# Performance work log

Measured on AMD Instinct MI355X. Metric: run time of the kernel, lower is better.

## Reference

```python
import jax, jax.numpy as jnp
import numpy as np


def setup_inputs() -> dict:
    key = jax.random.key(0)
    kq, kk, kv = jax.random.split(key, 3)
    B, L, E = 16, 2048, 512
    return {
        "queries": jax.random.normal(kq, (B, L, E), dtype=jnp.float32),
        "keys": jax.random.normal(kk, (B, L, E), dtype=jnp.float32),
        "values": jax.random.normal(kv, (B, L, E), dtype=jnp.float32),
    }


def reference(queries, keys, values):
    # queries: [B, L, E], keys: [B, S, E], values: [B, S, D]; causal mask requires L == S
    B, L, E = queries.shape
    S = keys.shape[1]
    scale = 1.0 / np.float32(np.sqrt(E))  # self.scale is None -> 1/sqrt(E)
    scores = jnp.einsum('ble,bse->bls', queries, keys)  # [B, L, S]
    causal = jnp.triu(jnp.ones((L, S), dtype=bool), k=1)  # True above diagonal -> masked
    scores = jnp.where(causal, -jnp.inf, scores)
    A = jax.nn.softmax(scale * scores, axis=-1)  # dropout p=0.0 -> identity
    V = jnp.einsum('bls,bsd->bld', A, values)  # [B, L, D]
    return V
```

## Files before the change

### kernel.cpp

```cpp
#include <hip/hip_runtime.h>
#include <hip/hip_bf16.h>

typedef __attribute__((ext_vector_type(8))) short short8;
typedef __attribute__((ext_vector_type(4))) float f32x4;
typedef __attribute__((ext_vector_type(4))) unsigned short us4;

#define L_ 2048
#define E_ 512
#define SCALE 0.04419417382415922f

static __device__ __forceinline__ unsigned short f2bf(float f) {
  return __builtin_bit_cast(unsigned short, __float2bfloat16(f));
}
static __device__ __forceinline__ float bf2f(unsigned short u) {
  return __builtin_bit_cast(float, (unsigned)u << 16);
}

__global__ void
__launch_bounds__(512)
__attribute__((amdgpu_waves_per_eu(2, 2)))
fattn_kernel(const float* __restrict__ Q,
             const float* __restrict__ K,
             const float* __restrict__ V,
             float* __restrict__ O) {
  __shared__ us4 Sp[4][2][4][2][64];
  __shared__ unsigned short P2[8][64][8];
  __shared__ float m_s[64], l_s[64], corr_s[64];

  const int tid  = threadIdx.x;
  const int w    = tid >> 6;
  const int lane = tid & 63;
  const int g    = lane >> 4;
  const int ln   = lane & 15;
  const int we   = w >> 1;
  const int ws   = w & 1;
  const int bid  = (int)blockIdx.x;
  const int bz   = bid & 15;
  const int q0   = (31 - (bid >> 4)) * 64;

  const float* Qb = Q + (size_t)bz * (L_ * E_);
  const float* Kb = K + (size_t)bz * (L_ * E_);
  const float* Vb = V + (size_t)bz * (L_ * E_);

  if (tid < 64) { m_s[tid] = -1e30f; l_s[tid] = 0.f; }

  short8 qf[4][4];
#pragma unroll
  for (int mt = 0; mt < 4; ++mt) {
    const float* qp = Qb + (size_t)(q0 + mt * 16 + ln) * E_ + (we * 128 + g * 8);
#pragma unroll
    for (int kc = 0; kc < 4; ++kc) {
      f32x4 a = *(const f32x4*)(qp + kc * 32);
      f32x4 b = *(const f32x4*)(qp + kc * 32 + 4);
      short8 t;
      t[0] = (short)f2bf(a[0] * SCALE); t[1] = (short)f2bf(a[1] * SCALE);
      t[2] = (short)f2bf(a[2] * SCALE); t[3] = (short)f2bf(a[3] * SCALE);
      t[4] = (short)f2bf(b[0] * SCALE); t[5] = (short)f2bf(b[1] * SCALE);
      t[6] = (short)f2bf(b[2] * SCALE); t[7] = (short)f2bf(b[3] * SCALE);
      qf[mt][kc] = t;
    }
  }

  f32x4 acc[4][4];
#pragma unroll
  for (int mt = 0; mt < 4; ++mt)
#pragma unroll
    for (int n = 0; n < 4; ++n) acc[mt][n] = (f32x4){0.f, 0.f, 0.f, 0.f};

  const int nIter = q0 / 64 + 1;
  for (int it = 0; it < nIter; ++it) {
    const int s0 = it * 64;

    float vr0[4][8];
#pragma unroll
    for (int n = 0; n < 4; ++n) {
      const float* vp = Vb + (size_t)(s0 + g * 8) * E_ + (w * 64 + n * 16 + ln);
#pragma unroll
      for (int i = 0; i < 8; ++i) vr0[n][i] = vp[(size_t)i * E_];
    }

#pragma unroll
    for (int nt = 0; nt < 2; ++nt) {
      f32x4 ps[4];
#pragma unroll
      for (int mt = 0; mt < 4; ++mt) ps[mt] = (f32x4){0.f, 0.f, 0.f, 0.f};
      const float* kp = Kb + (size_t)(s0 + ws * 32 + nt * 16 + ln) * E_ + (we * 128 + g * 8);
#pragma unroll
      for (int kc = 0; kc < 4; ++kc) {
        f32x4 a = *(const f32x4*)(kp + kc * 32);
        f32x4 b = *(const f32x4*)(kp + kc * 32 + 4);
        short8 kf;
        kf[0] = (short)f2bf(a[0]); kf[1] = (short)f2bf(a[1]);
        kf[2] = (short)f2bf(a[2]); kf[3] = (short)f2bf(a[3]);
        kf[4] = (short)f2bf(b[0]); kf[5] = (short)f2bf(b[1]);
        kf[6] = (short)f2bf(b[2]); kf[7] = (short)f2bf(b[3]);
#pragma unroll
        for (int mt = 0; mt < 4; ++mt)
          ps[mt] = __builtin_amdgcn_mfma_f32_16x16x32_bf16(qf[mt][kc], kf, ps[mt], 0, 0, 0);
      }
#pragma unroll
      for (int mt = 0; mt < 4; ++mt) {
        us4 u;
        u[0] = f2bf(ps[mt][0]); u[1] = f2bf(ps[mt][1]);
        u[2] = f2bf(ps[mt][2]); u[3] = f2bf(ps[mt][3]);
        Sp[we][ws][mt][nt][lane] = u;
      }
    }
    __syncthreads();

    if (w < 4) {
      const int mt = w;
      float p[4][4];
#pragma unroll
      for (int j = 0; j < 4; ++j) {
        us4 u0 = Sp[0][j >> 1][mt][j & 1][lane];
        us4 u1 = Sp[1][j >> 1][mt][j & 1][lane];
        us4 u2 = Sp[2][j >> 1][mt][j & 1][lane];
        us4 u3 = Sp[3][j >> 1][mt][j & 1][lane];
#pragma unroll
        for (int r = 0; r < 4; ++r)
          p[j][r] = bf2f(u0[r]) + bf2f(u1[r]) + bf2f(u2[r]) + bf2f(u3[r]);
      }
      if (s0 + 63 > q0) {
#pragma unroll
        for (int j = 0; j < 4; ++j)
#pragma unroll
          for (int r = 0; r < 4; ++r)
            if (s0 + j * 16 + ln > q0 + mt * 16 + g * 4 + r) p[j][r] = -1e30f;
      }
      float tmax[4], lsum[4];
#pragma unroll
      for (int r = 0; r < 4; ++r)
        tmax[r] = fmaxf(fmaxf(p[0][r], p[1][r]), fmaxf(p[2][r], p[3][r]));
#pragma unroll
      for (int off = 1; off < 16; off <<= 1)
#pragma unroll
        for (int r = 0; r < 4; ++r) tmax[r] = fmaxf(tmax[r], __shfl_xor(tmax[r], off));
      f32x4 mr = *(const f32x4*)&m_s[mt * 16 + g * 4];
      float mnew[4], corr[4];
#pragma unroll
      for (int r = 0; r < 4; ++r) {
        mnew[r] = fmaxf(mr[r], tmax[r]);
        corr[r] = __expf(mr[r] - mnew[r]);
        lsum[r] = 0.f;
      }
#pragma unroll
      for (int j = 0; j < 4; ++j)
#pragma unroll
        for (int r = 0; r < 4; ++r) {
          p[j][r] = __expf(p[j][r] - mnew[r]);
          lsum[r] += p[j][r];
        }
#pragma unroll
      for (int off = 1; off < 16; off <<= 1)
#pragma unroll
        for (int r = 0; r < 4; ++r) lsum[r] += __shfl_xor(lsum[r], off);
      if (ln == 0) {
#pragma unroll
        for (int r = 0; r < 4; ++r) {
          const int q = mt * 16 + g * 4 + r;
          m_s[q] = mnew[r];
          corr_s[q] = corr[r];
          l_s[q] = l_s[q] * corr[r] + lsum[r];
        }
      }
#pragma unroll
      for (int j = 0; j < 4; ++j)
#pragma unroll
        for (int r = 0; r < 4; ++r) {
          const int s = j * 16 + ln;
          P2[s >> 3][mt * 16 + g * 4 + r][s & 7] = f2bf(p[j][r]);
        }
    }
    __syncthreads();

    float vr1[4][8];
#pragma unroll
    for (int n = 0; n < 4; ++n) {
      const float* vp = Vb + (size_t)(s0 + 32 + g * 8) * E_ + (w * 64 + n * 16 + ln);
#pragma unroll
      for (int i = 0; i < 8; ++i) vr1[n][i] = vp[(size_t)i * E_];
    }
    short8 vf0[4];
#pragma unroll
    for (int n = 0; n < 4; ++n) {
      short8 t;
#pragma unroll
      for (int i = 0; i < 8; ++i) t[i] = (short)f2bf(vr0[n][i]);
      vf0[n] = t;
    }
#pragma unroll
    for (int mt = 0; mt < 4; ++mt) {
      f32x4 c4 = *(const f32x4*)&corr_s[mt * 16 + g * 4];
#pragma unroll
      for (int n = 0; n < 4; ++n) {
        acc[mt][n][0] *= c4[0]; acc[mt][n][1] *= c4[1];
        acc[mt][n][2] *= c4[2]; acc[mt][n][3] *= c4[3];
      }
    }
    {
      short8 pa[4];
#pragma unroll
      for (int mt = 0; mt < 4; ++mt)
        pa[mt] = *(const short8*)&P2[g][mt * 16 + ln][0];
#pragma unroll
      for (int n = 0; n < 4; ++n)
#pragma unroll
        for (int mt = 0; mt < 4; ++mt)
          acc[mt][n] = __builtin_amdgcn_mfma_f32_16x16x32_bf16(pa[mt], vf0[n], acc[mt][n], 0, 0, 0);
    }
    {
      short8 vf1[4];
#pragma unroll
      for (int n = 0; n < 4; ++n) {
        short8 t;
#pragma unroll
        for (int i = 0; i < 8; ++i) t[i] = (short)f2bf(vr1[n][i]);
        vf1[n] = t;
      }
      short8 pa[4];
#pragma unroll
      for (int mt = 0; mt < 4; ++mt)
        pa[mt] = *(const short8*)&P2[4 + g][mt * 16 + ln][0];
#pragma unroll
      for (int n = 0; n < 4; ++n)
#pragma unroll
        for (int mt = 0; mt < 4; ++mt)
          acc[mt][n] = __builtin_amdgcn_mfma_f32_16x16x32_bf16(pa[mt], vf1[n], acc[mt][n], 0, 0, 0);
    }
  }

  float* Ob = O + (size_t)bz * (L_ * E_);
#pragma unroll
  for (int mt = 0; mt < 4; ++mt) {
    f32x4 lv = *(const f32x4*)&l_s[mt * 16 + g * 4];
    float inv[4];
#pragma unroll
    for (int r = 0; r < 4; ++r) inv[r] = 1.0f / lv[r];
#pragma unroll
    for (int n = 0; n < 4; ++n) {
      const int col = w * 64 + n * 16 + ln;
#pragma unroll
      for (int r = 0; r < 4; ++r)
        Ob[(size_t)(q0 + mt * 16 + g * 4 + r) * E_ + col] = acc[mt][n][r] * inv[r];
    }
  }
}

extern "C" void kernel_launch(void* const* d_in, const int* in_sizes, int n_in,
                              void* d_out, int out_size, void* d_ws, size_t ws_size,
                              hipStream_t stream) {
  const float* Q = (const float*)d_in[0];
  const float* K = (const float*)d_in[1];
  const float* V = (const float*)d_in[2];
  float* O = (float*)d_out;
  fattn_kernel<<<dim3(512), 512, 0, stream>>>(Q, K, V, O);
}
```

Baseline: 247.5 us.

## Halve query tile to 32 rows, double grid and raise occupancy

```diff
diff --git a/kernel.cpp b/kernel.cpp
--- a/kernel.cpp
+++ b/kernel.cpp
@@ -17,15 +17,14 @@
 }
 
 __global__ void
-__launch_bounds__(512)
-__attribute__((amdgpu_waves_per_eu(2, 2)))
+__launch_bounds__(512, 4)
 fattn_kernel(const float* __restrict__ Q,
              const float* __restrict__ K,
              const float* __restrict__ V,
              float* __restrict__ O) {
-  __shared__ us4 Sp[4][2][4][2][64];
-  __shared__ unsigned short P2[8][64][8];
-  __shared__ float m_s[64], l_s[64], corr_s[64];
+  __shared__ us4 Sp[4][2][2][2][64];
+  __shared__ unsigned short P2[8][32][8];
+  __shared__ float m_s[32], l_s[32], corr_s[32];
 
   const int tid  = threadIdx.x;
   const int w    = tid >> 6;
@@ -36,17 +35,17 @@
   const int ws   = w & 1;
   const int bid  = (int)blockIdx.x;
   const int bz   = bid & 15;
-  const int q0   = (31 - (bid >> 4)) * 64;
+  const int q0   = (63 - (bid >> 4)) * 32;
 
   const float* Qb = Q + (size_t)bz * (L_ * E_);
   const float* Kb = K + (size_t)bz * (L_ * E_);
   const float* Vb = V + (size_t)bz * (L_ * E_);
 
-  if (tid < 64) { m_s[tid] = -1e30f; l_s[tid] = 0.f; }
-
-  short8 qf[4][4];
-#pragma unroll
-  for (int mt = 0; mt < 4; ++mt) {
+  if (tid < 32) { m_s[tid] = -1e30f; l_s[tid] = 0.f; }
+
+  short8 qf[2][4];
+#pragma unroll
+  for (int mt = 0; mt < 2; ++mt) {
     const float* qp = Qb + (size_t)(q0 + mt * 16 + ln) * E_ + (we * 128 + g * 8);
 #pragma unroll
     for (int kc = 0; kc < 4; ++kc) {
@@ -61,9 +60,9 @@
     }
   }
 
-  f32x4 acc[4][4];
-#pragma unroll
-  for (int mt = 0; mt < 4; ++mt)
+  f32x4 acc[2][4];
+#pragma unroll
+  for (int mt = 0; mt < 2; ++mt)
 #pragma unroll
     for (int n = 0; n < 4; ++n) acc[mt][n] = (f32x4){0.f, 0.f, 0.f, 0.f};
 
@@ -71,19 +70,11 @@
   for (int it = 0; it < nIter; ++it) {
     const int s0 = it * 64;
 
-    float vr0[4][8];
-#pragma unroll
-    for (int n = 0; n < 4; ++n) {
-      const float* vp = Vb + (size_t)(s0 + g * 8) * E_ + (w * 64 + n * 16 + ln);
-#pragma unroll
-      for (int i = 0; i < 8; ++i) vr0[n][i] = vp[(size_t)i * E_];
-    }
-
 #pragma unroll
     for (int nt = 0; nt < 2; ++nt) {
-      f32x4 ps[4];
-#pragma unroll
-      for (int mt = 0; mt < 4; ++mt) ps[mt] = (f32x4){0.f, 0.f, 0.f, 0.f};
+      f32x4 ps[2];
+      ps[0] = (f32x4){0.f, 0.f, 0.f, 0.f};
+      ps[1] = (f32x4){0.f, 0.f, 0.f, 0.f};
       const float* kp = Kb + (size_t)(s0 + ws * 32 + nt * 16 + ln) * E_ + (we * 128 + g * 8);
 #pragma unroll
       for (int kc = 0; kc < 4; ++kc) {
@@ -95,11 +86,11 @@
         kf[4] = (short)f2bf(b[0]); kf[5] = (short)f2bf(b[1]);
         kf[6] = (short)f2bf(b[2]); kf[7] = (short)f2bf(b[3]);
 #pragma unroll
-        for (int mt = 0; mt < 4; ++mt)
+        for (int mt = 0; mt < 2; ++mt)
           ps[mt] = __builtin_amdgcn_mfma_f32_16x16x32_bf16(qf[mt][kc], kf, ps[mt], 0, 0, 0);
       }
 #pragma unroll
-      for (int mt = 0; mt < 4; ++mt) {
+      for (int mt = 0; mt < 2; ++mt) {
         us4 u;
         u[0] = f2bf(ps[mt][0]); u[1] = f2bf(ps[mt][1]);
         u[2] = f2bf(ps[mt][2]); u[3] = f2bf(ps[mt][3]);
@@ -108,7 +99,7 @@
     }
     __syncthreads();
 
-    if (w < 4) {
+    if (w < 2) {
       const int mt = w;
       float p[4][4];
 #pragma unroll
@@ -174,23 +165,8 @@
     }
     __syncthreads();
 
-    float vr1[4][8];
-#pragma unroll
-    for (int n = 0; n < 4; ++n) {
-      const float* vp = Vb + (size_t)(s0 + 32 + g * 8) * E_ + (w * 64 + n * 16 + ln);
-#pragma unroll
-      for (int i = 0; i < 8; ++i) vr1[n][i] = vp[(size_t)i * E_];
-    }
-    short8 vf0[4];
-#pragma unroll
-    for (int n = 0; n < 4; ++n) {
-      short8 t;
-#pragma unroll
-      for (int i = 0; i < 8; ++i) t[i] = (short)f2bf(vr0[n][i]);
-      vf0[n] = t;
-    }
-#pragma unroll
-    for (int mt = 0; mt < 4; ++mt) {
+#pragma unroll
+    for (int mt = 0; mt < 2; ++mt) {
       f32x4 c4 = *(const f32x4*)&corr_s[mt * 16 + g * 4];
 #pragma unroll
       for (int n = 0; n < 4; ++n) {
@@ -198,41 +174,33 @@
         acc[mt][n][2] *= c4[2]; acc[mt][n][3] *= c4[3];
       }
     }
-    {
-      short8 pa[4];
-#pragma unroll
-      for (int mt = 0; mt < 4; ++mt)
-        pa[mt] = *(const short8*)&P2[g][mt * 16 + ln][0];
-#pragma unroll
-      for (int n = 0; n < 4; ++n)
-#pragma unroll
-        for (int mt = 0; mt < 4; ++mt)
-          acc[mt][n] = __builtin_amdgcn_mfma_f32_16x16x32_bf16(pa[mt], vf0[n], acc[mt][n], 0, 0, 0);
-    }
-    {
-      short8 vf1[4];
+#pragma unroll
+    for (int h = 0; h < 2; ++h) {
+      float vr[4][8];
 #pragma unroll
       for (int n = 0; n < 4; ++n) {
-        short8 t;
-#pragma unroll
-        for (int i = 0; i < 8; ++i) t[i] = (short)f2bf(vr1[n][i]);
-        vf1[n] = t;
-      }
-      short8 pa[4];
-#pragma unroll
-      for (int mt = 0; mt < 4; ++mt)
-        pa[mt] = *(const short8*)&P2[4 + g][mt * 16 + ln][0];
-#pragma unroll
-      for (int n = 0; n < 4; ++n)
-#pragma unroll
-        for (int mt = 0; mt < 4; ++mt)
-          acc[mt][n] = __builtin_amdgcn_mfma_f32_16x16x32_bf16(pa[mt], vf1[n], acc[mt][n], 0, 0, 0);
+        const float* vp = Vb + (size_t)(s0 + h * 32 + g * 8) * E_ + (w * 64 + n * 16 + ln);
+#pragma unroll
+        for (int i = 0; i < 8; ++i) vr[n][i] = vp[(size_t)i * E_];
+      }
+      short8 pa[2];
+      pa[0] = *(const short8*)&P2[h * 4 + g][ln][0];
+      pa[1] = *(const short8*)&P2[h * 4 + g][16 + ln][0];
+#pragma unroll
+      for (int n = 0; n < 4; ++n) {
+        short8 vf;
+#pragma unroll
+        for (int i = 0; i < 8; ++i) vf[i] = (short)f2bf(vr[n][i]);
+#pragma unroll
+        for (int mt = 0; mt < 2; ++mt)
+          acc[mt][n] = __builtin_amdgcn_mfma_f32_16x16x32_bf16(pa[mt], vf, acc[mt][n], 0, 0, 0);
+      }
     }
   }
 
   float* Ob = O + (size_t)bz * (L_ * E_);
 #pragma unroll
-  for (int mt = 0; mt < 4; ++mt) {
+  for (int mt = 0; mt < 2; ++mt) {
     f32x4 lv = *(const f32x4*)&l_s[mt * 16 + g * 4];
     float inv[4];
 #pragma unroll
@@ -254,5 +222,5 @@
   const float* K = (const float*)d_in[1];
   const float* V = (const float*)d_in[2];
   float* O = (float*)d_out;
-  fattn_kernel<<<dim3(512), 512, 0, stream>>>(Q, K, V, O);
-}
+  fattn_kernel<<<dim3(1024), 512, 0, stream>>>(Q, K, V, O);
+}
```

Measured after the change: 381.4 us. 1.54x slower.
